# Performance work log

Hardware: AMD Instinct MI355X
Metric: run time of the kernel (lower is better)

## Reference

```python
import jax, jax.numpy as jnp
import numpy as np

N = 100000
E = 1600000
IN_DIM = 64
EMB_DIM = 64
BN_EPS = 1e-5


def setup_inputs() -> dict:
    key = jax.random.key(0)
    ks = jax.random.split(key, 8)
    x = jax.random.normal(ks[0], (N, IN_DIM), dtype=jnp.float32)
    edge_index = jax.random.randint(ks[1], (2, E), 0, N, dtype=jnp.int64)
    # GIN learned epsilon (train_eps=True), initialized to 0 as in PyG
    eps = jnp.zeros((), dtype=jnp.float32)
    # MLP params: Linear(in, emb) -> BN -> ReLU -> Linear(emb, emb)
    s1 = 1.0 / np.sqrt(IN_DIM)
    W1 = jax.random.uniform(ks[2], (IN_DIM, EMB_DIM), jnp.float32, -s1, s1)
    b1 = jax.random.uniform(ks[3], (EMB_DIM,), jnp.float32, -s1, s1)
    gamma = jnp.ones((EMB_DIM,), jnp.float32)
    beta = jnp.zeros((EMB_DIM,), jnp.float32)
    s2 = 1.0 / np.sqrt(EMB_DIM)
    W2 = jax.random.uniform(ks[4], (EMB_DIM, EMB_DIM), jnp.float32, -s2, s2)
    b2 = jax.random.uniform(ks[5], (EMB_DIM,), jnp.float32, -s2, s2)
    return {"x": x, "edge_index": edge_index, "eps": eps,
            "W1": W1, "b1": b1, "gamma": gamma, "beta": beta,
            "W2": W2, "b2": b2}


def reference(x, edge_index, eps, W1, b1, gamma, beta, W2, b2):
    src, dst = edge_index[0], edge_index[1]
    # GIN aggregation: sum of neighbor (source) features at each destination
    agg = jax.ops.segment_sum(x[src], dst, num_segments=N)  # [N, IN_DIM]
    h = (1.0 + eps) * x + agg
    # MLP: Linear -> BatchNorm1d (training-mode batch stats) -> ReLU -> Linear
    h1 = h @ W1 + b1                                   # [N, EMB_DIM]
    mean = jnp.mean(h1, axis=0)
    var = jnp.mean((h1 - mean) ** 2, axis=0)           # biased var, as torch BN
    h1n = (h1 - mean) * jax.lax.rsqrt(var + BN_EPS) * gamma + beta
    h2 = jax.nn.relu(h1n)
    return h2 @ W2 + b2                                # [N, EMB_DIM]
```

## Files before the change

kernel.cpp:

```cpp
#include <hip/hip_runtime.h>

#define NNODES 100000
#define NEDGES 1600000
#define DIM 64
#define NB 782
#define NPB 256
#define CHUNK 6250
#define CAP 3968
#define HP 68
#define NTILES 6250

typedef __attribute__((ext_vector_type(4))) float f32x4;
typedef __attribute__((ext_vector_type(8))) short s16x8;

__device__ __forceinline__ unsigned short bf16_rne(float f) {
  unsigned u = __float_as_uint(f);
  u += 0x7FFF + ((u >> 16) & 1);
  return (unsigned short)(u >> 16);
}
__device__ __forceinline__ float bf16_to_f32(unsigned short h) {
  return __uint_as_float(((unsigned)h) << 16);
}

__global__ __launch_bounds__(256) void prep_kernel(
    const float* __restrict__ x, unsigned short* __restrict__ xb,
    int* __restrict__ gcursor, float* __restrict__ sums,
    const float* __restrict__ W1, const float* __restrict__ W2,
    unsigned short* __restrict__ Wp1, unsigned short* __restrict__ Wp2) {
  int i = blockIdx.x * 256 + threadIdx.x;
  float4 v = ((const float4*)x)[i];
  ushort4 o;
  o.x = bf16_rne(v.x); o.y = bf16_rne(v.y);
  o.z = bf16_rne(v.z); o.w = bf16_rne(v.w);
  ((ushort4*)xb)[i] = o;
  if (blockIdx.x == 0) {
    int t = threadIdx.x;
    for (int b = t; b < NB; b += 256) gcursor[b] = b * CAP;
    if (t < 2 * DIM) sums[t] = 0.0f;
    if (t < 128) {
      int lane = t & 63;
      const float* W = (t >= 64) ? W2 : W1;
      unsigned short* Wp = (t >= 64) ? Wp2 : Wp1;
      int q = lane >> 4, n16 = lane & 15;
#pragma unroll
      for (int f = 0; f < 8; ++f) {
        int kk = f >> 2, nt = f & 3;
#pragma unroll
        for (int j = 0; j < 8; ++j) {
          int k = kk * 32 + q * 8 + j;
          int n = nt * 16 + n16;
          Wp[f * 512 + lane * 8 + j] = bf16_rne(W[k * DIM + n]);
        }
      }
    }
  }
}

__global__ __launch_bounds__(1024) void partition_kernel(
    const int* __restrict__ ei, int* __restrict__ gcursor,
    int* __restrict__ bpart) {
  __shared__ int sd[1024];
  __shared__ int delta[1024];
  __shared__ int lcur[1024];
  __shared__ int stage[CHUNK];
  __shared__ unsigned short sbuck[CHUNK];
  int t = threadIdx.x;
  sd[t] = 0;
  __syncthreads();
  int base = blockIdx.x * CHUNK;
  for (int i = t; i < CHUNK; i += 1024)
    atomicAdd(&sd[ei[NEDGES + base + i] >> 7], 1);
  __syncthreads();
  int v = sd[t];
  for (int off = 1; off < 1024; off <<= 1) {
    int a = (t >= off) ? sd[t - off] : 0;
    __syncthreads();
    sd[t] += a;
    __syncthreads();
  }
  int excl = sd[t] - v;
  delta[t] = (v ? atomicAdd(&gcursor[t], v) : 0) - excl;
  lcur[t] = excl;
  __syncthreads();
  for (int i = t; i < CHUNK; i += 1024) {
    int s = ei[base + i];
    int d = ei[NEDGES + base + i];
    int b = d >> 7;
    int p = atomicAdd(&lcur[b], 1);
    stage[p] = ((d & 127) << 17) | s;
    sbuck[p] = (unsigned short)b;
  }
  __syncthreads();
  for (int i = t; i < CHUNK; i += 1024)
    bpart[delta[sbuck[i]] + i] = stage[i];
}

__global__ __launch_bounds__(512) void mega_kernel(
    const int* __restrict__ bpart, const int* __restrict__ gcursor,
    const unsigned short* __restrict__ xb, float* __restrict__ h1,
    const unsigned short* __restrict__ Wp, const float* __restrict__ b1,
    const float* __restrict__ epsp,
    float* __restrict__ sums, float* __restrict__ sumsq) {
  __shared__ int sd[128];
  __shared__ int cur[128];
  __shared__ int stage[CAP];
  __shared__ unsigned short hbuf[128 * HP];
  __shared__ float lsum[DIM];
  __shared__ float lsq[DIM];
  int b = blockIdx.x;
  int t = threadIdx.x;
  if (t < 128) sd[t] = 0;
  if (t < DIM) { lsum[t] = 0.0f; lsq[t] = 0.0f; }
  __syncthreads();
  int pbase = b * CAP;
  int cnt = gcursor[b] - pbase;
  for (int i = t; i < cnt; i += 512)
    atomicAdd(&sd[bpart[pbase + i] >> 17], 1);
  __syncthreads();
  int deg = (t < 128) ? sd[t] : 0;
  for (int off = 1; off < 128; off <<= 1) {
    int a = (t < 128 && t >= off) ? sd[t - off] : 0;
    __syncthreads();
    if (t < 128) sd[t] += a;
    __syncthreads();
  }
  if (t < 128) cur[t] = sd[t] - deg;
  __syncthreads();
  for (int i = t; i < cnt; i += 512) {
    int v = bpart[pbase + i];
    int p = atomicAdd(&cur[v >> 17], 1);
    stage[p] = v & 0x1FFFF;
  }
  __syncthreads();
  {
    int part = t & 15;
    int ng = t >> 4;
#pragma unroll 1
    for (int pass = 0; pass < 4; ++pass) {
      int nl = ng + pass * 32;
      int e0 = (nl == 0) ? 0 : sd[nl - 1];
      int e1 = sd[nl];
      float4 a0 = make_float4(0.f, 0.f, 0.f, 0.f);
      float4 a1 = a0, a2 = a0, a3 = a0;
      int e = e0;
      for (; e + 4 <= e1; e += 4) {
        int s0 = stage[e + 0];
        int s1 = stage[e + 1];
        int s2 = stage[e + 2];
        int s3 = stage[e + 3];
        ushort4 u0 = ((const ushort4*)(xb + (size_t)s0 * DIM))[part];
        ushort4 u1 = ((const ushort4*)(xb + (size_t)s1 * DIM))[part];
        ushort4 u2 = ((const ushort4*)(xb + (size_t)s2 * DIM))[part];
        ushort4 u3 = ((const ushort4*)(xb + (size_t)s3 * DIM))[part];
        a0.x += bf16_to_f32(u0.x); a0.y += bf16_to_f32(u0.y);
        a0.z += bf16_to_f32(u0.z); a0.w += bf16_to_f32(u0.w);
        a1.x += bf16_to_f32(u1.x); a1.y += bf16_to_f32(u1.y);
        a1.z += bf16_to_f32(u1.z); a1.w += bf16_to_f32(u1.w);
        a2.x += bf16_to_f32(u2.x); a2.y += bf16_to_f32(u2.y);
        a2.z += bf16_to_f32(u2.z); a2.w += bf16_to_f32(u2.w);
        a3.x += bf16_to_f32(u3.x); a3.y += bf16_to_f32(u3.y);
        a3.z += bf16_to_f32(u3.z); a3.w += bf16_to_f32(u3.w);
      }
      for (; e < e1; ++e) {
        int s = stage[e];
        ushort4 u = ((const ushort4*)(xb + (size_t)s * DIM))[part];
        a0.x += bf16_to_f32(u.x); a0.y += bf16_to_f32(u.y);
        a0.z += bf16_to_f32(u.z); a0.w += bf16_to_f32(u.w);
      }
      ushort4 o;
      o.x = bf16_rne((a0.x + a1.x) + (a2.x + a3.x));
      o.y = bf16_rne((a0.y + a1.y) + (a2.y + a3.y));
      o.z = bf16_rne((a0.z + a1.z) + (a2.z + a3.z));
      o.w = bf16_rne((a0.w + a1.w) + (a2.w + a3.w));
      *(ushort4*)&hbuf[nl * HP + part * 4] = o;
    }
  }
  __syncthreads();
  {
    int wave = t >> 6;
    int lane = t & 63;
    int tile = b * 8 + wave;
    if (tile < NTILES) {
      int q = lane >> 4;
      int r16 = lane & 15;
      float onep = 1.0f + epsp[0];
      s16x8 bf[8];
#pragma unroll
      for (int f = 0; f < 8; ++f)
        bf[f] = ((const s16x8*)Wp)[f * 64 + lane];
      int lrow = wave * 16 + r16;
      int grow = b * 128 + lrow;
      const s16x8* xrow = (const s16x8*)(xb + (size_t)grow * DIM);
      f32x4 acc[4] = {{0.f,0.f,0.f,0.f},{0.f,0.f,0.f,0.f},
                      {0.f,0.f,0.f,0.f},{0.f,0.f,0.f,0.f}};
#pragma unroll
      for (int kk = 0; kk < 2; ++kk) {
        s16x8 xv = xrow[kk * 4 + q];
        const unsigned short* hb = &hbuf[lrow * HP + kk * 32 + q * 8];
        ushort4 h0 = *(const ushort4*)hb;
        ushort4 h4 = *(const ushort4*)(hb + 4);
        s16x8 a;
        a[0] = (short)bf16_rne(fmaf(onep, bf16_to_f32((unsigned short)xv[0]), bf16_to_f32(h0.x)));
        a[1] = (short)bf16_rne(fmaf(onep, bf16_to_f32((unsigned short)xv[1]), bf16_to_f32(h0.y)));
        a[2] = (short)bf16_rne(fmaf(onep, bf16_to_f32((unsigned short)xv[2]), bf16_to_f32(h0.z)));
        a[3] = (short)bf16_rne(fmaf(onep, bf16_to_f32((unsigned short)xv[3]), bf16_to_f32(h0.w)));
        a[4] = (short)bf16_rne(fmaf(onep, bf16_to_f32((unsigned short)xv[4]), bf16_to_f32(h4.x)));
        a[5] = (short)bf16_rne(fmaf(onep, bf16_to_f32((unsigned short)xv[5]), bf16_to_f32(h4.y)));
        a[6] = (short)bf16_rne(fmaf(onep, bf16_to_f32((unsigned short)xv[6]), bf16_to_f32(h4.z)));
        a[7] = (short)bf16_rne(fmaf(onep, bf16_to_f32((unsigned short)xv[7]), bf16_to_f32(h4.w)));
#pragma unroll
        for (int nt = 0; nt < 4; ++nt)
          acc[nt] = __builtin_amdgcn_mfma_f32_16x16x32_bf16(
              a, bf[kk * 4 + nt], acc[nt], 0, 0, 0);
      }
      int orow = tile * 16 + q * 4;
#pragma unroll
      for (int nt = 0; nt < 4; ++nt) {
        int col = nt * 16 + r16;
        float bb = b1[col];
        float sl = 0.0f, ql = 0.0f;
#pragma unroll
        for (int r = 0; r < 4; ++r) {
          float v = acc[nt][r] + bb;
          h1[(size_t)(orow + r) * DIM + col] = v;
          sl += v;
          ql = fmaf(v, v, ql);
        }
        sl += __shfl_down(sl, 32); ql += __shfl_down(ql, 32);
        sl += __shfl_down(sl, 16); ql += __shfl_down(ql, 16);
        if (q == 0) {
          atomicAdd(&lsum[col], sl);
          atomicAdd(&lsq[col], ql);
        }
      }
    }
  }
  __syncthreads();
  if (t < DIM) {
    atomicAdd(&sums[t], lsum[t]);
    atomicAdd(&sumsq[t], lsq[t]);
  }
}

__global__ __launch_bounds__(256) void fused2_kernel(
    const float* __restrict__ h1, float* __restrict__ out,
    const unsigned short* __restrict__ Wp, const float* __restrict__ b2,
    const float* __restrict__ gamma, const float* __restrict__ beta,
    const float* __restrict__ sums, const float* __restrict__ sumsq) {
  __shared__ float sc_s[DIM];
  __shared__ float sh_s[DIM];
  int t = threadIdx.x;
  if (t < DIM) {
    float invN = 1.0f / (float)NNODES;
    float m = sums[t] * invN;
    float v = fmaf(-m, m, sumsq[t] * invN);
    float sc = gamma[t] * rsqrtf(v + 1e-5f);
    sc_s[t] = sc;
    sh_s[t] = fmaf(-m, sc, beta[t]);
  }
  __syncthreads();
  int wave = t >> 6;
  int lane = t & 63;
  int tile = blockIdx.x * 4 + wave;
  if (tile >= NTILES) return;
  int q = lane >> 4;
  int r16 = lane & 15;
  s16x8 bf[8];
#pragma unroll
  for (int f = 0; f < 8; ++f)
    bf[f] = ((const s16x8*)Wp)[f * 64 + lane];
  int arow = tile * 16 + r16;
  const float* hr = h1 + (size_t)arow * DIM + q * 8;
  f32x4 acc[4] = {{0.f,0.f,0.f,0.f},{0.f,0.f,0.f,0.f},
                  {0.f,0.f,0.f,0.f},{0.f,0.f,0.f,0.f}};
#pragma unroll
  for (int kk = 0; kk < 2; ++kk) {
    int kbase = kk * 32 + q * 8;
    float4 hv0 = *(const float4*)(hr + kk * 32);
    float4 hv1 = *(const float4*)(hr + kk * 32 + 4);
    float4 sc0 = *(const float4*)(sc_s + kbase);
    float4 sc1 = *(const float4*)(sc_s + kbase + 4);
    float4 sh0 = *(const float4*)(sh_s + kbase);
    float4 sh1 = *(const float4*)(sh_s + kbase + 4);
    s16x8 a;
    a[0] = (short)bf16_rne(fmaxf(fmaf(hv0.x, sc0.x, sh0.x), 0.f));
    a[1] = (short)bf16_rne(fmaxf(fmaf(hv0.y, sc0.y, sh0.y), 0.f));
    a[2] = (short)bf16_rne(fmaxf(fmaf(hv0.z, sc0.z, sh0.z), 0.f));
    a[3] = (short)bf16_rne(fmaxf(fmaf(hv0.w, sc0.w, sh0.w), 0.f));
    a[4] = (short)bf16_rne(fmaxf(fmaf(hv1.x, sc1.x, sh1.x), 0.f));
    a[5] = (short)bf16_rne(fmaxf(fmaf(hv1.y, sc1.y, sh1.y), 0.f));
    a[6] = (short)bf16_rne(fmaxf(fmaf(hv1.z, sc1.z, sh1.z), 0.f));
    a[7] = (short)bf16_rne(fmaxf(fmaf(hv1.w, sc1.w, sh1.w), 0.f));
#pragma unroll
    for (int nt = 0; nt < 4; ++nt)
      acc[nt] = __builtin_amdgcn_mfma_f32_16x16x32_bf16(
          a, bf[kk * 4 + nt], acc[nt], 0, 0, 0);
  }
  int orow = tile * 16 + q * 4;
#pragma unroll
  for (int nt = 0; nt < 4; ++nt) {
    int col = nt * 16 + r16;
    float bb = b2[col];
#pragma unroll
    for (int r = 0; r < 4; ++r)
      out[(size_t)(orow + r) * DIM + col] = acc[nt][r] + bb;
  }
}

extern "C" void kernel_launch(void* const* d_in, const int* in_sizes, int n_in,
                              void* d_out, int out_size, void* d_ws, size_t ws_size,
                              hipStream_t stream) {
  (void)in_sizes; (void)n_in; (void)out_size; (void)ws_size;
  const float* x     = (const float*)d_in[0];
  const int*   ei    = (const int*)d_in[1];
  const float* eps   = (const float*)d_in[2];
  const float* W1    = (const float*)d_in[3];
  const float* b1    = (const float*)d_in[4];
  const float* gamma = (const float*)d_in[5];
  const float* beta  = (const float*)d_in[6];
  const float* W2    = (const float*)d_in[7];
  const float* b2    = (const float*)d_in[8];
  float* outp = (float*)d_out;

  const int N = NNODES;

  float* h1      = (float*)d_ws;
  float* sums    = h1 + (size_t)N * DIM;
  float* sumsq   = sums + DIM;
  int*   gcursor = (int*)(sumsq + DIM);
  unsigned short* Wp1 = (unsigned short*)(gcursor + ((NB + 1) & ~1));
  unsigned short* Wp2 = Wp1 + 4096;
  int*            bpart = (int*)d_out;
  unsigned short* xb    = (unsigned short*)d_out + (size_t)NB * CAP * 2;

  prep_kernel     <<<N * DIM / 4 / 256, 256, 0, stream>>>(x, xb, gcursor, sums,
                                                          W1, W2, Wp1, Wp2);
  partition_kernel<<<NPB, 1024, 0, stream>>>(ei, gcursor, bpart);
  mega_kernel     <<<NB, 512, 0, stream>>>(bpart, gcursor, xb, h1,
                                           Wp1, b1, eps, sums, sumsq);
  fused2_kernel   <<<(NTILES + 3) / 4, 256, 0, stream>>>(h1, outp, Wp2, b2,
                                                         gamma, beta, sums, sumsq);
}
```

Before: 175.7 us.

## Fuse prep into partition kernel, use wave-shuffle scans, widen gather loads, slice BN atomics

Merges the bf16 conversion and weight packing into the edge partition kernel and replaces the initialization with a memset, removing one kernel launch. The LDS-based Hillis-Steele prefix scans become wave shuffle scans, so far fewer barriers are needed. The neighbor gather now uses 16-byte loads: two half-groups each take alternate edges and are combined with a shuffle. hbuf padding changes to 72 so rows stay aligned for the wider accesses. BatchNorm sum atomics are spread across 32 slices to cut contention, at the cost of a small reduction in the final kernel.

Result: faster. 159.4 us (median of 2 runs) (-9.3%).

```diff
diff --git a/kernel.cpp b/kernel.cpp
--- a/kernel.cpp
+++ b/kernel.cpp
@@ -7,8 +7,9 @@
 #define NPB 256
 #define CHUNK 6250
 #define CAP 3968
-#define HP 68
+#define HP 72
 #define NTILES 6250
+#define NSLICE 32
 
 typedef __attribute__((ext_vector_type(4))) float f32x4;
 typedef __attribute__((ext_vector_type(8))) short s16x8;
@@ -22,64 +23,72 @@
   return __uint_as_float(((unsigned)h) << 16);
 }
 
-__global__ __launch_bounds__(256) void prep_kernel(
+__global__ __launch_bounds__(1024) void prep_part_kernel(
     const float* __restrict__ x, unsigned short* __restrict__ xb,
-    int* __restrict__ gcursor, float* __restrict__ sums,
+    const int* __restrict__ ei, int* __restrict__ gcursor,
+    int* __restrict__ bpart,
     const float* __restrict__ W1, const float* __restrict__ W2,
     unsigned short* __restrict__ Wp1, unsigned short* __restrict__ Wp2) {
-  int i = blockIdx.x * 256 + threadIdx.x;
-  float4 v = ((const float4*)x)[i];
-  ushort4 o;
-  o.x = bf16_rne(v.x); o.y = bf16_rne(v.y);
-  o.z = bf16_rne(v.z); o.w = bf16_rne(v.w);
-  ((ushort4*)xb)[i] = o;
-  if (blockIdx.x == 0) {
-    int t = threadIdx.x;
-    for (int b = t; b < NB; b += 256) gcursor[b] = b * CAP;
-    if (t < 2 * DIM) sums[t] = 0.0f;
-    if (t < 128) {
-      int lane = t & 63;
-      const float* W = (t >= 64) ? W2 : W1;
-      unsigned short* Wp = (t >= 64) ? Wp2 : Wp1;
-      int q = lane >> 4, n16 = lane & 15;
-#pragma unroll
-      for (int f = 0; f < 8; ++f) {
-        int kk = f >> 2, nt = f & 3;
-#pragma unroll
-        for (int j = 0; j < 8; ++j) {
-          int k = kk * 32 + q * 8 + j;
-          int n = nt * 16 + n16;
-          Wp[f * 512 + lane * 8 + j] = bf16_rne(W[k * DIM + n]);
-        }
-      }
-    }
-  }
-}
-
-__global__ __launch_bounds__(1024) void partition_kernel(
-    const int* __restrict__ ei, int* __restrict__ gcursor,
-    int* __restrict__ bpart) {
   __shared__ int sd[1024];
   __shared__ int delta[1024];
   __shared__ int lcur[1024];
+  __shared__ int wsum[16];
   __shared__ int stage[CHUNK];
   __shared__ unsigned short sbuck[CHUNK];
   int t = threadIdx.x;
   sd[t] = 0;
+  for (int i = blockIdx.x * 1024 + t; i < NNODES * DIM / 4; i += NPB * 1024) {
+    float4 v = ((const float4*)x)[i];
+    ushort4 o;
+    o.x = bf16_rne(v.x); o.y = bf16_rne(v.y);
+    o.z = bf16_rne(v.z); o.w = bf16_rne(v.w);
+    ((ushort4*)xb)[i] = o;
+  }
+  if (blockIdx.x == 0 && t < 128) {
+    int lane = t & 63;
+    const float* W = (t >= 64) ? W2 : W1;
+    unsigned short* Wp = (t >= 64) ? Wp2 : Wp1;
+    int q = lane >> 4, n16 = lane & 15;
+#pragma unroll
+    for (int f = 0; f < 8; ++f) {
+      int kk = f >> 2, nt = f & 3;
+#pragma unroll
+      for (int j = 0; j < 8; ++j) {
+        int k = kk * 32 + q * 8 + j;
+        int n = nt * 16 + n16;
+        Wp[f * 512 + lane * 8 + j] = bf16_rne(W[k * DIM + n]);
+      }
+    }
+  }
   __syncthreads();
   int base = blockIdx.x * CHUNK;
   for (int i = t; i < CHUNK; i += 1024)
     atomicAdd(&sd[ei[NEDGES + base + i] >> 7], 1);
   __syncthreads();
   int v = sd[t];
-  for (int off = 1; off < 1024; off <<= 1) {
-    int a = (t >= off) ? sd[t - off] : 0;
-    __syncthreads();
-    sd[t] += a;
-    __syncthreads();
-  }
-  int excl = sd[t] - v;
-  delta[t] = (v ? atomicAdd(&gcursor[t], v) : 0) - excl;
+  int lane = t & 63;
+  int incl = v;
+#pragma unroll
+  for (int off = 1; off < 64; off <<= 1) {
+    int n = __shfl_up(incl, off);
+    if (lane >= off) incl += n;
+  }
+  if (lane == 63) wsum[t >> 6] = incl;
+  __syncthreads();
+  if (t < 16) {
+    int w = wsum[t];
+#pragma unroll
+    for (int off = 1; off < 16; off <<= 1) {
+      int n = __shfl_up(w, off);
+      if (t >= off) w += n;
+    }
+    wsum[t] = w;
+  }
+  __syncthreads();
+  int wid = t >> 6;
+  if (wid) incl += wsum[wid - 1];
+  int excl = incl - v;
+  delta[t] = (v ? (t * CAP + atomicAdd(&gcursor[t], v)) : 0) - excl;
   lcur[t] = excl;
   __syncthreads();
   for (int i = t; i < CHUNK; i += 1024) {
@@ -100,11 +109,12 @@
     const unsigned short* __restrict__ xb, float* __restrict__ h1,
     const unsigned short* __restrict__ Wp, const float* __restrict__ b1,
     const float* __restrict__ epsp,
-    float* __restrict__ sums, float* __restrict__ sumsq) {
+    float* __restrict__ sums32, float* __restrict__ sumsq32) {
   __shared__ int sd[128];
   __shared__ int cur[128];
+  __shared__ int swv[2];
   __shared__ int stage[CAP];
-  __shared__ unsigned short hbuf[128 * HP];
+  __shared__ __align__(16) unsigned short hbuf[128 * HP];
   __shared__ float lsum[DIM];
   __shared__ float lsq[DIM];
   int b = blockIdx.x;
@@ -113,18 +123,27 @@
   if (t < DIM) { lsum[t] = 0.0f; lsq[t] = 0.0f; }
   __syncthreads();
   int pbase = b * CAP;
-  int cnt = gcursor[b] - pbase;
+  int cnt = gcursor[b];
   for (int i = t; i < cnt; i += 512)
     atomicAdd(&sd[bpart[pbase + i] >> 17], 1);
   __syncthreads();
-  int deg = (t < 128) ? sd[t] : 0;
-  for (int off = 1; off < 128; off <<= 1) {
-    int a = (t < 128 && t >= off) ? sd[t - off] : 0;
-    __syncthreads();
-    if (t < 128) sd[t] += a;
-    __syncthreads();
-  }
-  if (t < 128) cur[t] = sd[t] - deg;
+  int deg = 0, incl = 0;
+  if (t < 128) {
+    deg = sd[t];
+    incl = deg;
+#pragma unroll
+    for (int off = 1; off < 64; off <<= 1) {
+      int n = __shfl_up(incl, off);
+      if ((t & 63) >= off) incl += n;
+    }
+    if ((t & 63) == 63) swv[t >> 6] = incl;
+  }
+  __syncthreads();
+  if (t < 128) {
+    if (t >= 64) incl += swv[0];
+    sd[t] = incl;
+    cur[t] = incl - deg;
+  }
   __syncthreads();
   for (int i = t; i < cnt; i += 512) {
     int v = bpart[pbase + i];
@@ -133,46 +152,67 @@
   }
   __syncthreads();
   {
-    int part = t & 15;
+    int part = t & 7;
+    int half = (t >> 3) & 1;
     int ng = t >> 4;
 #pragma unroll 1
     for (int pass = 0; pass < 4; ++pass) {
       int nl = ng + pass * 32;
       int e0 = (nl == 0) ? 0 : sd[nl - 1];
       int e1 = sd[nl];
-      float4 a0 = make_float4(0.f, 0.f, 0.f, 0.f);
-      float4 a1 = a0, a2 = a0, a3 = a0;
+      f32x4 aA0 = {0.f,0.f,0.f,0.f}, aA1 = aA0, aB0 = aA0, aB1 = aA0;
       int e = e0;
-      for (; e + 4 <= e1; e += 4) {
-        int s0 = stage[e + 0];
-        int s1 = stage[e + 1];
-        int s2 = stage[e + 2];
-        int s3 = stage[e + 3];
-        ushort4 u0 = ((const ushort4*)(xb + (size_t)s0 * DIM))[part];
-        ushort4 u1 = ((const ushort4*)(xb + (size_t)s1 * DIM))[part];
-        ushort4 u2 = ((const ushort4*)(xb + (size_t)s2 * DIM))[part];
-        ushort4 u3 = ((const ushort4*)(xb + (size_t)s3 * DIM))[part];
-        a0.x += bf16_to_f32(u0.x); a0.y += bf16_to_f32(u0.y);
-        a0.z += bf16_to_f32(u0.z); a0.w += bf16_to_f32(u0.w);
-        a1.x += bf16_to_f32(u1.x); a1.y += bf16_to_f32(u1.y);
-        a1.z += bf16_to_f32(u1.z); a1.w += bf16_to_f32(u1.w);
-        a2.x += bf16_to_f32(u2.x); a2.y += bf16_to_f32(u2.y);
-        a2.z += bf16_to_f32(u2.z); a2.w += bf16_to_f32(u2.w);
-        a3.x += bf16_to_f32(u3.x); a3.y += bf16_to_f32(u3.y);
-        a3.z += bf16_to_f32(u3.z); a3.w += bf16_to_f32(u3.w);
-      }
-      for (; e < e1; ++e) {
+      for (; e + 8 <= e1; e += 8) {
+        int s0 = stage[e + 0 + half];
+        int s1 = stage[e + 2 + half];
+        int s2 = stage[e + 4 + half];
+        int s3 = stage[e + 6 + half];
+        s16x8 u0 = *(const s16x8*)(xb + (size_t)s0 * DIM + part * 8);
+        s16x8 u1 = *(const s16x8*)(xb + (size_t)s1 * DIM + part * 8);
+        s16x8 u2 = *(const s16x8*)(xb + (size_t)s2 * DIM + part * 8);
+        s16x8 u3 = *(const s16x8*)(xb + (size_t)s3 * DIM + part * 8);
+#pragma unroll
+        for (int j = 0; j < 4; ++j) {
+          aA0[j] += bf16_to_f32((unsigned short)u0[j]) +
+                    bf16_to_f32((unsigned short)u2[j]);
+          aA1[j] += bf16_to_f32((unsigned short)u0[j + 4]) +
+                    bf16_to_f32((unsigned short)u2[j + 4]);
+          aB0[j] += bf16_to_f32((unsigned short)u1[j]) +
+                    bf16_to_f32((unsigned short)u3[j]);
+          aB1[j] += bf16_to_f32((unsigned short)u1[j + 4]) +
+                    bf16_to_f32((unsigned short)u3[j + 4]);
+        }
+      }
+      for (; e + 2 <= e1; e += 2) {
+        int s = stage[e + half];
+        s16x8 u = *(const s16x8*)(xb + (size_t)s * DIM + part * 8);
+#pragma unroll
+        for (int j = 0; j < 4; ++j) {
+          aA0[j] += bf16_to_f32((unsigned short)u[j]);
+          aA1[j] += bf16_to_f32((unsigned short)u[j + 4]);
+        }
+      }
+      if (e < e1 && half == 0) {
         int s = stage[e];
-        ushort4 u = ((const ushort4*)(xb + (size_t)s * DIM))[part];
-        a0.x += bf16_to_f32(u.x); a0.y += bf16_to_f32(u.y);
-        a0.z += bf16_to_f32(u.z); a0.w += bf16_to_f32(u.w);
-      }
-      ushort4 o;
-      o.x = bf16_rne((a0.x + a1.x) + (a2.x + a3.x));
-      o.y = bf16_rne((a0.y + a1.y) + (a2.y + a3.y));
-      o.z = bf16_rne((a0.z + a1.z) + (a2.z + a3.z));
-      o.w = bf16_rne((a0.w + a1.w) + (a2.w + a3.w));
-      *(ushort4*)&hbuf[nl * HP + part * 4] = o;
+        s16x8 u = *(const s16x8*)(xb + (size_t)s * DIM + part * 8);
+#pragma unroll
+        for (int j = 0; j < 4; ++j) {
+          aA0[j] += bf16_to_f32((unsigned short)u[j]);
+          aA1[j] += bf16_to_f32((unsigned short)u[j + 4]);
+        }
+      }
+      float r[8];
+#pragma unroll
+      for (int j = 0; j < 4; ++j) {
+        r[j] = aA0[j] + aB0[j];
+        r[j + 4] = aA1[j] + aB1[j];
+      }
+      s16x8 o;
+#pragma unroll
+      for (int j = 0; j < 8; ++j)
+        o[j] = (short)bf16_rne(r[j] + __shfl_down(r[j], 8));
+      if (half == 0)
+        *(s16x8*)&hbuf[nl * HP + part * 8] = o;
     }
   }
   __syncthreads();
@@ -196,18 +236,13 @@
 #pragma unroll
       for (int kk = 0; kk < 2; ++kk) {
         s16x8 xv = xrow[kk * 4 + q];
-        const unsigned short* hb = &hbuf[lrow * HP + kk * 32 + q * 8];
-        ushort4 h0 = *(const ushort4*)hb;
-        ushort4 h4 = *(const ushort4*)(hb + 4);
+        s16x8 hv = *(const s16x8*)&hbuf[lrow * HP + kk * 32 + q * 8];
         s16x8 a;
-        a[0] = (short)bf16_rne(fmaf(onep, bf16_to_f32((unsigned short)xv[0]), bf16_to_f32(h0.x)));
-        a[1] = (short)bf16_rne(fmaf(onep, bf16_to_f32((unsigned short)xv[1]), bf16_to_f32(h0.y)));
-        a[2] = (short)bf16_rne(fmaf(onep, bf16_to_f32((unsigned short)xv[2]), bf16_to_f32(h0.z)));
-        a[3] = (short)bf16_rne(fmaf(onep, bf16_to_f32((unsigned short)xv[3]), bf16_to_f32(h0.w)));
-        a[4] = (short)bf16_rne(fmaf(onep, bf16_to_f32((unsigned short)xv[4]), bf16_to_f32(h4.x)));
-        a[5] = (short)bf16_rne(fmaf(onep, bf16_to_f32((unsigned short)xv[5]), bf16_to_f32(h4.y)));
-        a[6] = (short)bf16_rne(fmaf(onep, bf16_to_f32((unsigned short)xv[6]), bf16_to_f32(h4.z)));
-        a[7] = (short)bf16_rne(fmaf(onep, bf16_to_f32((unsigned short)xv[7]), bf16_to_f32(h4.w)));
+#pragma unroll
+        for (int j = 0; j < 8; ++j)
+          a[j] = (short)bf16_rne(fmaf(onep,
+                     bf16_to_f32((unsigned short)xv[j]),
+                     bf16_to_f32((unsigned short)hv[j])));
 #pragma unroll
         for (int nt = 0; nt < 4; ++nt)
           acc[nt] = __builtin_amdgcn_mfma_f32_16x16x32_bf16(
@@ -237,8 +272,9 @@
   }
   __syncthreads();
   if (t < DIM) {
-    atomicAdd(&sums[t], lsum[t]);
-    atomicAdd(&sumsq[t], lsq[t]);
+    int sl = (b & (NSLICE - 1)) * DIM;
+    atomicAdd(&sums32[sl + t], lsum[t]);
+    atomicAdd(&sumsq32[sl + t], lsq[t]);
   }
 }
 
@@ -246,14 +282,20 @@
     const float* __restrict__ h1, float* __restrict__ out,
     const unsigned short* __restrict__ Wp, const float* __restrict__ b2,
     const float* __restrict__ gamma, const float* __restrict__ beta,
-    const float* __restrict__ sums, const float* __restrict__ sumsq) {
+    const float* __restrict__ sums32, const float* __restrict__ sumsq32) {
   __shared__ float sc_s[DIM];
   __shared__ float sh_s[DIM];
   int t = threadIdx.x;
   if (t < DIM) {
+    float s = 0.0f, q2 = 0.0f;
+#pragma unroll
+    for (int j = 0; j < NSLICE; ++j) {
+      s  += sums32[j * DIM + t];
+      q2 += sumsq32[j * DIM + t];
+    }
     float invN = 1.0f / (float)NNODES;
-    float m = sums[t] * invN;
-    float v = fmaf(-m, m, sumsq[t] * invN);
+    float m = s * invN;
+    float v = fmaf(-m, m, q2 * invN);
     float sc = gamma[t] * rsqrtf(v + 1e-5f);
     sc_s[t] = sc;
     sh_s[t] = fmaf(-m, sc, beta[t]);
@@ -324,20 +366,23 @@
 
   const int N = NNODES;
 
-  float* h1      = (float*)d_ws;
-  float* sums    = h1 + (size_t)N * DIM;
-  float* sumsq   = sums + DIM;
-  int*   gcursor = (int*)(sumsq + DIM);
-  unsigned short* Wp1 = (unsigned short*)(gcursor + ((NB + 1) & ~1));
+  float* h1       = (float*)d_ws;
+  float* sums32   = h1 + (size_t)N * DIM;
+  float* sumsq32  = sums32 + NSLICE * DIM;
+  int*   gcursor  = (int*)(sumsq32 + NSLICE * DIM);
+  unsigned short* Wp1 = (unsigned short*)(gcursor + 1024);
   unsigned short* Wp2 = Wp1 + 4096;
   int*            bpart = (int*)d_out;
   unsigned short* xb    = (unsigned short*)d_out + (size_t)NB * CAP * 2;
 
-  prep_kernel     <<<N * DIM / 4 / 256, 256, 0, stream>>>(x, xb, gcursor, sums,
-                                                          W1, W2, Wp1, Wp2);
-  partition_kernel<<<NPB, 1024, 0, stream>>>(ei, gcursor, bpart);
+  hipMemsetAsync(sums32, 0,
+                 (size_t)(2 * NSLICE * DIM) * sizeof(float) + 1024 * sizeof(int),
+                 stream);
+  prep_part_kernel<<<NPB, 1024, 0, stream>>>(x, xb, ei, gcursor, bpart,
+                                             W1, W2, Wp1, Wp2);
   mega_kernel     <<<NB, 512, 0, stream>>>(bpart, gcursor, xb, h1,
-                                           Wp1, b1, eps, sums, sumsq);
+                                           Wp1, b1, eps, sums32, sumsq32);
   fused2_kernel   <<<(NTILES + 3) / 4, 256, 0, stream>>>(h1, outp, Wp2, b2,
-                                                         gamma, beta, sums, sumsq);
-}
+                                                         gamma, beta,
+                                                         sums32, sumsq32);
+}
```
